# Kernel optimization log

Measured on AMD Instinct MI355X. Metric: run time of the kernel, lower is better.

## Reference

```python
import jax, jax.numpy as jnp
import numpy as np

T, B = 1024, 16384
GAMMA = 0.99
LAMBDA = 0.97


def setup_inputs() -> dict:
    key = jax.random.key(0)
    k1, k2 = jax.random.split(key)
    value = jax.random.normal(k1, (T + 1, B), dtype=jnp.float32)
    reward = jax.random.normal(k2, (T, B), dtype=jnp.float32)
    return {"value": value, "reward": reward}


def reference(value, reward):
    # delta[t] = r[t] + gamma * V[t+1] - V[t]          shape (T, B)
    delta = reward + GAMMA * value[1:] - value[:-1]
    coef = jnp.float32(GAMMA * LAMBDA)

    def step(carry, d):
        adv_t = d + coef * carry
        return adv_t, adv_t

    init = jnp.zeros(delta.shape[1:], dtype=delta.dtype)
    # reverse-in-time scan: adv[t] = delta[t] + gamma*lambda * adv[t+1]
    _, adv = jax.lax.scan(step, init, delta, reverse=True)
    return adv
```

## Files before the change

kernel.cpp:

```cpp
#include <hip/hip_runtime.h>


constexpr int T_ = 1024;
constexpr int B_ = 16384;
constexpr int L_ = 16;
constexpr int C_ = T_ / L_;
constexpr float GAMMA = 0.99f;
constexpr float COEF  = (float)(0.99 * 0.97);

__host__ __device__ constexpr float pow_coef(int n) {
    float p = 1.0f;
    for (int i = 0; i < n; ++i) p *= COEF;
    return p;
}
constexpr float CL = pow_coef(L_);

__global__ __launch_bounds__(256) void gae_local(
    const float* __restrict__ value,
    const float* __restrict__ reward,
    float* __restrict__ S,
    float* __restrict__ out)
{
    const int c4    = blockIdx.x * 256 + threadIdx.x;
    const int chunk = blockIdx.y;
    const size_t b  = (size_t)c4 * 4;
    const int t0    = chunk * L_;

    float4 v[L_ + 1];
    float4 r[L_];
    #pragma unroll
    for (int i = 0; i <= L_; ++i)
        v[i] = *(const float4*)(value + (size_t)(t0 + i) * B_ + b);
    #pragma unroll
    for (int i = 0; i < L_; ++i)
        r[i] = *(const float4*)(reward + (size_t)(t0 + i) * B_ + b);

    float4 a = make_float4(0.f, 0.f, 0.f, 0.f);
    #pragma unroll
    for (int i = L_ - 1; i >= 0; --i) {
        a.x = (r[i].x + GAMMA * v[i + 1].x - v[i].x) + COEF * a.x;
        a.y = (r[i].y + GAMMA * v[i + 1].y - v[i].y) + COEF * a.y;
        a.z = (r[i].z + GAMMA * v[i + 1].z - v[i].z) + COEF * a.z;
        a.w = (r[i].w + GAMMA * v[i + 1].w - v[i].w) + COEF * a.w;
        *(float4*)(out + (size_t)(t0 + i) * B_ + b) = a;
    }
    *(float4*)(S + (size_t)chunk * B_ + b) = a;
}

__global__ __launch_bounds__(256) void gae_carry(float* __restrict__ S)
{
    const int col = blockIdx.x * 256 + threadIdx.x;

    float s[C_];
    #pragma unroll
    for (int j = 0; j < C_; ++j)
        s[j] = S[(size_t)j * B_ + col];

    float run = 0.f;
    #pragma unroll
    for (int j = C_ - 1; j >= 0; --j) {
        S[(size_t)j * B_ + col] = run;
        run = s[j] + CL * run;
    }
}

__global__ __launch_bounds__(256) void gae_fix(
    const float* __restrict__ S,
    float* __restrict__ out)
{
    const int c4    = blockIdx.x * 256 + threadIdx.x;
    const int chunk = blockIdx.y;
    const size_t b  = (size_t)c4 * 4;
    const int t0    = chunk * L_;

    float4 carry = *(const float4*)(S + (size_t)chunk * B_ + b);

    float4 o[L_];
    #pragma unroll
    for (int i = 0; i < L_; ++i)
        o[i] = *(const float4*)(out + (size_t)(t0 + i) * B_ + b);

    float p = COEF;
    #pragma unroll
    for (int i = L_ - 1; i >= 0; --i) {
        o[i].x += p * carry.x;
        o[i].y += p * carry.y;
        o[i].z += p * carry.z;
        o[i].w += p * carry.w;
        *(float4*)(out + (size_t)(t0 + i) * B_ + b) = o[i];
        p *= COEF;
    }
}

extern "C" void kernel_launch(void* const* d_in, const int* in_sizes, int n_in,
                              void* d_out, int out_size, void* d_ws, size_t ws_size,
                              hipStream_t stream) {
    const float* value  = (const float*)d_in[0];
    const float* reward = (const float*)d_in[1];
    float* out = (float*)d_out;
    float* S   = (float*)d_ws;

    dim3 block(256);
    dim3 gridA(B_ / 4 / 256, C_);
    dim3 gridC(B_ / 256);
    dim3 gridF(B_ / 4 / 256, C_ - 1);

    gae_local<<<gridA, block, 0, stream>>>(value, reward, S, out);
    gae_carry<<<gridC, block, 0, stream>>>(S);
    gae_fix  <<<gridF, block, 0, stream>>>(S, out);
}
```

Baseline: 190.7 us.

## Replace three-pass chunked scan with reduce-then-recompute using per-thread carry prefix

The local-scan, carry-propagation and fix-up kernels are replaced by two kernels. The first computes only per-chunk sums. The second recomputes each chunk's scan after folding the sums of later chunks into its starting carry, and writes the output once with nontemporal stores. This removes the read-modify-write pass over the output and one launch. In exchange, value and reward are read twice and each thread serially reads a variable number of chunk sums, which adds latency and imbalance across chunks.

After: 190.7 us. About the same (-0.0%).

```diff
diff --git a/kernel.cpp b/kernel.cpp
--- a/kernel.cpp
+++ b/kernel.cpp
@@ -15,10 +15,47 @@
 }
 constexpr float CL = pow_coef(L_);
 
-__global__ __launch_bounds__(256) void gae_local(
+typedef float f32x4 __attribute__((ext_vector_type(4)));
+
+static __device__ __forceinline__ void store_nt(float* p, float4 v) {
+    f32x4 nv = {v.x, v.y, v.z, v.w};
+    __builtin_nontemporal_store(nv, (f32x4*)p);
+}
+
+__global__ __launch_bounds__(256) void gae_sum(
     const float* __restrict__ value,
     const float* __restrict__ reward,
-    float* __restrict__ S,
+    float* __restrict__ S)
+{
+    const int c4    = blockIdx.x * 256 + threadIdx.x;
+    const int chunk = blockIdx.y;
+    const size_t b  = (size_t)c4 * 4;
+    const int t0    = chunk * L_;
+
+    float4 v[L_ + 1];
+    float4 r[L_];
+    #pragma unroll
+    for (int i = 0; i <= L_; ++i)
+        v[i] = *(const float4*)(value + (size_t)(t0 + i) * B_ + b);
+    #pragma unroll
+    for (int i = 0; i < L_; ++i)
+        r[i] = *(const float4*)(reward + (size_t)(t0 + i) * B_ + b);
+
+    float4 s = make_float4(0.f, 0.f, 0.f, 0.f);
+    #pragma unroll
+    for (int i = L_ - 1; i >= 0; --i) {
+        s.x = (r[i].x + GAMMA * v[i + 1].x - v[i].x) + COEF * s.x;
+        s.y = (r[i].y + GAMMA * v[i + 1].y - v[i].y) + COEF * s.y;
+        s.z = (r[i].z + GAMMA * v[i + 1].z - v[i].z) + COEF * s.z;
+        s.w = (r[i].w + GAMMA * v[i + 1].w - v[i].w) + COEF * s.w;
+    }
+    *(float4*)(S + (size_t)chunk * B_ + b) = s;
+}
+
+__global__ __launch_bounds__(256) void gae_out(
+    const float* __restrict__ value,
+    const float* __restrict__ reward,
+    const float* __restrict__ S,
     float* __restrict__ out)
 {
     const int c4    = blockIdx.x * 256 + threadIdx.x;
@@ -36,59 +73,21 @@
         r[i] = *(const float4*)(reward + (size_t)(t0 + i) * B_ + b);
 
     float4 a = make_float4(0.f, 0.f, 0.f, 0.f);
+    for (int j = C_ - 1; j > chunk; --j) {
+        float4 s = *(const float4*)(S + (size_t)j * B_ + b);
+        a.x = s.x + CL * a.x;
+        a.y = s.y + CL * a.y;
+        a.z = s.z + CL * a.z;
+        a.w = s.w + CL * a.w;
+    }
+
     #pragma unroll
     for (int i = L_ - 1; i >= 0; --i) {
         a.x = (r[i].x + GAMMA * v[i + 1].x - v[i].x) + COEF * a.x;
         a.y = (r[i].y + GAMMA * v[i + 1].y - v[i].y) + COEF * a.y;
         a.z = (r[i].z + GAMMA * v[i + 1].z - v[i].z) + COEF * a.z;
         a.w = (r[i].w + GAMMA * v[i + 1].w - v[i].w) + COEF * a.w;
-        *(float4*)(out + (size_t)(t0 + i) * B_ + b) = a;
-    }
-    *(float4*)(S + (size_t)chunk * B_ + b) = a;
-}
-
-__global__ __launch_bounds__(256) void gae_carry(float* __restrict__ S)
-{
-    const int col = blockIdx.x * 256 + threadIdx.x;
-
-    float s[C_];
-    #pragma unroll
-    for (int j = 0; j < C_; ++j)
-        s[j] = S[(size_t)j * B_ + col];
-
-    float run = 0.f;
-    #pragma unroll
-    for (int j = C_ - 1; j >= 0; --j) {
-        S[(size_t)j * B_ + col] = run;
-        run = s[j] + CL * run;
-    }
-}
-
-__global__ __launch_bounds__(256) void gae_fix(
-    const float* __restrict__ S,
-    float* __restrict__ out)
-{
-    const int c4    = blockIdx.x * 256 + threadIdx.x;
-    const int chunk = blockIdx.y;
-    const size_t b  = (size_t)c4 * 4;
-    const int t0    = chunk * L_;
-
-    float4 carry = *(const float4*)(S + (size_t)chunk * B_ + b);
-
-    float4 o[L_];
-    #pragma unroll
-    for (int i = 0; i < L_; ++i)
-        o[i] = *(const float4*)(out + (size_t)(t0 + i) * B_ + b);
-
-    float p = COEF;
-    #pragma unroll
-    for (int i = L_ - 1; i >= 0; --i) {
-        o[i].x += p * carry.x;
-        o[i].y += p * carry.y;
-        o[i].z += p * carry.z;
-        o[i].w += p * carry.w;
-        *(float4*)(out + (size_t)(t0 + i) * B_ + b) = o[i];
-        p *= COEF;
+        store_nt(out + (size_t)(t0 + i) * B_ + b, a);
     }
 }
 
@@ -101,11 +100,8 @@
     float* S   = (float*)d_ws;
 
     dim3 block(256);
-    dim3 gridA(B_ / 4 / 256, C_);
-    dim3 gridC(B_ / 256);
-    dim3 gridF(B_ / 4 / 256, C_ - 1);
+    dim3 grid(B_ / 4 / 256, C_);
 
-    gae_local<<<gridA, block, 0, stream>>>(value, reward, S, out);
-    gae_carry<<<gridC, block, 0, stream>>>(S);
-    gae_fix  <<<gridF, block, 0, stream>>>(S, out);
+    gae_sum<<<grid, block, 0, stream>>>(value, reward, S);
+    gae_out<<<grid, block, 0, stream>>>(value, reward, S, out);
 }
```
